# Performance work log

Hardware: AMD Instinct MI355X
Metric: run time of the kernel (lower is better)

The kernel has to match this reference:

```python
import jax, jax.numpy as jnp
import numpy as np

N_EMBED = 1024
HEAD_SIZE = 64
BLOCK_SIZE = 2048

def setup_inputs() -> dict:
    key = jax.random.key(0)
    kx, kq, kk, kv = jax.random.split(key, 4)
    scale = N_EMBED ** -0.5
    x = jax.random.normal(kx, (8, 2048, N_EMBED), dtype=jnp.float32)
    # nn.Linear weights stored as [out, in]; we keep [in, out] for x @ W
    Wq = jax.random.normal(kq, (N_EMBED, HEAD_SIZE), dtype=jnp.float32) * scale
    Wk = jax.random.normal(kk, (N_EMBED, HEAD_SIZE), dtype=jnp.float32) * scale
    Wv = jax.random.normal(kv, (N_EMBED, HEAD_SIZE), dtype=jnp.float32) * scale
    return {"x": x, "Wq": Wq, "Wk": Wk, "Wv": Wv}

def reference(x, Wq, Wk, Wv):
    B, T, C = x.shape
    q = x @ Wq  # [B,T,H]
    k = x @ Wk
    v = x @ Wv
    # NOTE: original scales by C**-0.5 (n_embed), not head_size**-0.5
    wei = jnp.einsum('bth,bsh->bts', q, k) * (C ** -0.5)  # [B,T,T]
    causal = jnp.tril(jnp.ones((T, T), dtype=bool))
    wei = jnp.where(causal, wei, -jnp.inf)
    wei = jax.nn.softmax(wei, axis=-1)
    out = jnp.einsum('bts,bsh->bth', wei, v)  # [B,T,H]
    return out
```

## Files before the change

### kernel.cpp

```cpp
#include <hip/hip_runtime.h>

#define B_ 8
#define T_ 2048
#define C_ 1024
#define H_ 64

typedef __attribute__((ext_vector_type(8))) short short8;
typedef __attribute__((ext_vector_type(4))) float floatx4;
typedef __attribute__((ext_vector_type(4))) int intx4;

static __device__ __forceinline__ unsigned short f2bf(float f) {
  unsigned int u = __builtin_bit_cast(unsigned int, f);
  u += 0x7FFFu + ((u >> 16) & 1u);
  return (unsigned short)(u >> 16);
}
static __device__ __forceinline__ unsigned short f2bf_t(float f) {
  return (unsigned short)(__builtin_bit_cast(unsigned int, f) >> 16);
}
static __device__ __forceinline__ float bf2f(unsigned short u) {
  return __builtin_bit_cast(float, ((unsigned int)u) << 16);
}
static __device__ __forceinline__ unsigned int fbits(float f) {
  return __builtin_bit_cast(unsigned int, f);
}

typedef const __attribute__((address_space(1))) unsigned int* gp1_t;
typedef __attribute__((address_space(3))) unsigned int* lp3_t;
static __device__ __forceinline__ void gl_lds16(const void* g, void* l) {
  __builtin_amdgcn_global_load_lds((gp1_t)g, (lp3_t)l, 16, 0, 0);
}

__global__ __launch_bounds__(256) void conv_w(const float* __restrict__ wq,
    const float* __restrict__ wk, const float* __restrict__ wv,
    unsigned short* __restrict__ wf) {
  int c = blockIdx.x * 256 + threadIdx.x;
  int lane = c & 63;
  int t = c >> 6;
  int ng = t % 12;
  int kk = t / 12;
  int k0 = kk * 32 + (lane >> 4) * 8;
  int n = ng * 16 + (lane & 15);
  const float* src;
  int col;
  float scale = 1.0f;
  if (n < 64)       { src = wq; col = n;       scale = 0.03125f * 1.44269504088896340736f; }
  else if (n < 128) { src = wk; col = n - 64;  }
  else              { src = wv; col = n - 128; }
  unsigned short o[8];
#pragma unroll
  for (int j = 0; j < 8; ++j) o[j] = f2bf(src[(size_t)(k0 + j) * H_ + col] * scale);
  *(uint4*)&wf[(size_t)c * 8] = *(const uint4*)o;
}

__global__ __launch_bounds__(256, 4) void qkv_proj(
    const float* __restrict__ x, const unsigned short* __restrict__ wf,
    unsigned short* __restrict__ qo, unsigned short* __restrict__ kf,
    unsigned short* __restrict__ vf) {
  __shared__ float XL[2][4096];
  int tid = threadIdx.x;
  int wave = tid >> 6, lane = tid & 63;
  int lane4 = lane & 15, quad = lane >> 4;
  int m0 = blockIdx.x * 32;
  int ph0 = blockIdx.x & 7;

  auto stage_ph = [&](int phr, int buf) {
#pragma unroll
    for (int j = 0; j < 4; ++j) {
      int c = (wave * 4 + j) * 64 + lane;
      int r = c >> 5, pc = c & 31;
      int cl = (pc & ~7) | ((pc ^ (r & 7)) & 7);
      gl_lds16(&x[(size_t)(m0 + r) * C_ + phr * 128 + cl * 4], &XL[buf][c * 4]);
    }
  };

  floatx4 acc[2][3];
#pragma unroll
  for (int mt = 0; mt < 2; ++mt)
#pragma unroll
    for (int nt = 0; nt < 3; ++nt) acc[mt][nt] = (floatx4)0.0f;

  stage_ph(ph0, 0);
  __syncthreads();

  for (int ph = 0; ph < 8; ++ph) {
    int buf = ph & 1;
    if (ph < 7) stage_ph((ph + 1 + ph0) & 7, buf ^ 1);
    int phr = (ph + ph0) & 7;
#pragma unroll
    for (int sl = 0; sl < 4; ++sl) {
      int s = phr * 4 + sl;
      short8 b[3];
#pragma unroll
      for (int nt = 0; nt < 3; ++nt)
        b[nt] = *(const short8*)&wf[(size_t)(s * 12 + wave * 3 + nt) * 512 + lane * 8];
      short8 a[2];
#pragma unroll
      for (int mt = 0; mt < 2; ++mt) {
        int r = mt * 16 + lane4;
        int c0 = sl * 8 + quad * 2;
        int pc0 = (c0 & ~7) | ((c0 ^ (r & 7)) & 7);
        int pc1 = ((c0 + 1) & ~7) | (((c0 + 1) ^ (r & 7)) & 7);
        float4 f0 = *(const float4*)&XL[buf][r * 128 + pc0 * 4];
        float4 f1 = *(const float4*)&XL[buf][r * 128 + pc1 * 4];
        intx4 pk;
        pk[0] = (int)__builtin_amdgcn_perm(fbits(f0.y), fbits(f0.x), 0x07060302u);
        pk[1] = (int)__builtin_amdgcn_perm(fbits(f0.w), fbits(f0.z), 0x07060302u);
        pk[2] = (int)__builtin_amdgcn_perm(fbits(f1.y), fbits(f1.x), 0x07060302u);
        pk[3] = (int)__builtin_amdgcn_perm(fbits(f1.w), fbits(f1.z), 0x07060302u);
        a[mt] = __builtin_bit_cast(short8, pk);
      }
#pragma unroll
      for (int mt = 0; mt < 2; ++mt)
#pragma unroll
        for (int nt = 0; nt < 3; ++nt)
          acc[mt][nt] = __builtin_amdgcn_mfma_f32_16x16x32_bf16(a[mt], b[nt], acc[mt][nt], 0, 0, 0);
    }
    __syncthreads();
  }

  unsigned short* VTB = (unsigned short*)&XL[0][0];
  unsigned short* KB  = VTB + 5120;
#pragma unroll
  for (int mt = 0; mt < 2; ++mt)
#pragma unroll
    for (int nt = 0; nt < 3; ++nt) {
      int n = wave * 48 + nt * 16 + lane4;
#pragma unroll
      for (int rr = 0; rr < 4; ++rr) {
        unsigned short val = f2bf(acc[mt][nt][rr]);
        int lrow = mt * 16 + quad * 4 + rr;
        if (n < 64)       qo[(size_t)(m0 + lrow) * H_ + n] = val;
        else if (n < 128) KB[lrow * 72 + (n - 64)] = val;
        else              VTB[(n - 128) * 40 + lrow] = val;
      }
    }
  __syncthreads();
  {
    int bb = m0 >> 11, t0 = m0 & 2047;
    int st = t0 >> 6, off = t0 & 63;
    int ks = tid >> 7, ctl = (tid >> 6) & 1, ln = tid & 63;
    int ct = (off >> 4) + ctl;
    int tl = ctl * 16 + (ln & 15);
    int h0 = ks * 32 + (ln >> 4) * 8;
    uint4 kd = *(const uint4*)&KB[tl * 72 + h0];
    *(uint4*)&kf[((size_t)((bb * 32 + st) * 2 + ks) * 4 + ct) * 512 + ln * 8] = kd;
    int nt = tid >> 6, l4 = tid & 15, qs = (tid >> 4) & 3;
    int ksv = off >> 5;
    uint4 vd = *(const uint4*)&VTB[(nt * 16 + l4) * 40 + qs * 8];
    *(uint4*)&vf[((size_t)((bb * 32 + st) * 2 + ksv) * 4 + nt) * 512 + (tid & 63) * 8] = vd;
  }
}

__global__ __launch_bounds__(256) void attn(
    const unsigned short* __restrict__ qi, const unsigned short* __restrict__ Kf,
    const unsigned short* __restrict__ Vf, unsigned short* __restrict__ Op,
    float* __restrict__ lsum) {
  __shared__ unsigned short PL[4][16][72];

  int tid = threadIdx.x;
  int wave = tid >> 6, lane = tid & 63;
  int lane4 = lane & 15, quad = lane >> 4;
  int qt = 31 - (int)blockIdx.x;
  int b = blockIdx.y, split = blockIdx.z;
  int qb = qt * 64;
  int base = b * T_;

  int ntile = qt + 1;
  int sBeg = (split * ntile) >> 2;
  int sEnd = ((split + 1) * ntile) >> 2;

  short8 aq[2];
#pragma unroll
  for (int ks = 0; ks < 2; ++ks)
    aq[ks] = *(const short8*)&qi[(size_t)(base + qb + wave * 16 + lane4) * H_ + ks * 32 + quad * 8];

  float lrow[4];
  floatx4 o[4];
#pragma unroll
  for (int r = 0; r < 4; ++r) lrow[r] = 0.0f;
#pragma unroll
  for (int nt = 0; nt < 4; ++nt) o[nt] = (floatx4)0.0f;

  for (int st = sBeg; st < sEnd; ++st) {
    size_t tb = (size_t)(b * 32 + st) * 8;
    short8 bk[2][4], bv[2][4];
#pragma unroll
    for (int ks = 0; ks < 2; ++ks)
#pragma unroll
      for (int ct = 0; ct < 4; ++ct)
        bk[ks][ct] = *(const short8*)&Kf[(tb + ks * 4 + ct) * 512 + lane * 8];
#pragma unroll
    for (int ks = 0; ks < 2; ++ks)
#pragma unroll
      for (int nt = 0; nt < 4; ++nt)
        bv[ks][nt] = *(const short8*)&Vf[(tb + ks * 4 + nt) * 512 + lane * 8];

    floatx4 sacc[4];
#pragma unroll
    for (int ct = 0; ct < 4; ++ct) sacc[ct] = (floatx4)0.0f;
#pragma unroll
    for (int ks = 0; ks < 2; ++ks)
#pragma unroll
      for (int ct = 0; ct < 4; ++ct)
        sacc[ct] = __builtin_amdgcn_mfma_f32_16x16x32_bf16(aq[ks], bk[ks][ct], sacc[ct], 0, 0, 0);

    if (st == qt) {
#pragma unroll
      for (int ct = 0; ct < 4; ++ct)
#pragma unroll
        for (int r = 0; r < 4; ++r) {
          int qrow = wave * 16 + quad * 4 + r;
          int scol = ct * 16 + lane4;
          if (scol > qrow) sacc[ct][r] = -3.0e38f;
        }
    }

#pragma unroll
    for (int ct = 0; ct < 4; ++ct)
#pragma unroll
      for (int r = 0; r < 4; ++r) {
        float p = exp2f(sacc[ct][r] - 8.0f);
        lrow[r] += p;
        PL[wave][quad * 4 + r][ct * 16 + lane4] = f2bf_t(p);
      }

#pragma unroll
    for (int ks = 0; ks < 2; ++ks) {
      short8 pa = *(const short8*)&PL[wave][lane4][ks * 32 + quad * 8];
#pragma unroll
      for (int nt = 0; nt < 4; ++nt)
        o[nt] = __builtin_amdgcn_mfma_f32_16x16x32_bf16(pa, bv[ks][nt], o[nt], 0, 0, 0);
    }
  }

#pragma unroll
  for (int off = 1; off < 16; off <<= 1)
#pragma unroll
    for (int r = 0; r < 4; ++r) lrow[r] += __shfl_xor(lrow[r], off);

  size_t pbase = (((size_t)split * 8 + b) * 32 + qt) * 64;
#pragma unroll
  for (int r = 0; r < 4; ++r) {
    int row = wave * 16 + quad * 4 + r;
#pragma unroll
    for (int nt = 0; nt < 4; ++nt)
      Op[(pbase + row) * 64 + nt * 16 + lane4] = f2bf(o[nt][r]);
    if (lane4 == 0) lsum[pbase + row] = lrow[r];
  }
}

__global__ __launch_bounds__(256) void merge_splits(
    const unsigned short* __restrict__ Op, const float* __restrict__ lsum,
    float* __restrict__ out) {
  int idx = blockIdx.x * 256 + threadIdx.x;
  int row = idx >> 4;
  int h4 = (idx & 15) * 4;
  int b = row >> 11, t = row & 2047;
  int qt = t >> 6, r = t & 63;
  float O0 = 0.f, O1 = 0.f, O2 = 0.f, O3 = 0.f, l = 0.f;
#pragma unroll
  for (int s = 0; s < 4; ++s) {
    size_t p = (((size_t)s * 8 + b) * 32 + qt) * 64 + r;
    l += lsum[p];
    ushort4 ov = *(const ushort4*)&Op[p * 64 + h4];
    O0 += bf2f(ov.x); O1 += bf2f(ov.y); O2 += bf2f(ov.z); O3 += bf2f(ov.w);
  }
  float inv = 1.0f / l;
  float4 res = make_float4(O0 * inv, O1 * inv, O2 * inv, O3 * inv);
  *(float4*)&out[(size_t)row * H_ + h4] = res;
}

extern "C" void kernel_launch(void* const* d_in, const int* in_sizes, int n_in,
                              void* d_out, int out_size, void* d_ws, size_t ws_size,
                              hipStream_t stream) {
  const float* x  = (const float*)d_in[0];
  const float* wq = (const float*)d_in[1];
  const float* wk = (const float*)d_in[2];
  const float* wv = (const float*)d_in[3];
  float* out = (float*)d_out;

  char* ws = (char*)d_ws;
  unsigned short* wf = (unsigned short*)ws;
  unsigned short* qb = (unsigned short*)(ws + 393216);
  unsigned short* kf = (unsigned short*)(ws + 2490368);
  unsigned short* vf = (unsigned short*)(ws + 4587520);
  unsigned short* Op = (unsigned short*)(ws + 6684672);
  float*          ls = (float*)(ws + 15073280);

  conv_w<<<96, 256, 0, stream>>>(wq, wk, wv, wf);
  qkv_proj<<<512, 256, 0, stream>>>(x, wf, qb, kf, vf);
  attn<<<dim3(32, 8, 4), 256, 0, stream>>>(qb, kf, vf, Op, ls);
  merge_splits<<<1024, 256, 0, stream>>>(Op, ls, out);
}
```

Measured before the change: 130.3 us.

## Stage K/V tile pairs through LDS with register prefetch in attention

The attention kernel now loads K and V tiles cooperatively across the workgroup into shared memory, two tiles at a time. The next pair is prefetched into registers while the current pair is computed. Previously each wave loaded its own copies straight from global memory. The change also adds s_setprio around the MFMA sections and sets a launch bound of 3 blocks per CU. It adds two barriers per tile pair and more LDS and register pressure, which could reduce occupancy or force spills.

```diff
diff --git a/kernel.cpp b/kernel.cpp
--- a/kernel.cpp
+++ b/kernel.cpp
@@ -151,11 +151,12 @@
   }
 }
 
-__global__ __launch_bounds__(256) void attn(
+__global__ __launch_bounds__(256, 3) void attn(
     const unsigned short* __restrict__ qi, const unsigned short* __restrict__ Kf,
     const unsigned short* __restrict__ Vf, unsigned short* __restrict__ Op,
     float* __restrict__ lsum) {
-  __shared__ unsigned short PL[4][16][72];
+  __shared__ unsigned short KVS[2][8192];
+  __shared__ unsigned short PL[2][4][16][72];
 
   int tid = threadIdx.x;
   int wave = tid >> 6, lane = tid & 63;
@@ -181,28 +182,49 @@
 #pragma unroll
   for (int nt = 0; nt < 4; ++nt) o[nt] = (floatx4)0.0f;
 
-  for (int st = sBeg; st < sEnd; ++st) {
-    size_t tb = (size_t)(b * 32 + st) * 8;
-    short8 bk[2][4], bv[2][4];
+  uint4 rs[8];
+  auto stage_pair = [&](int t0) {
+#pragma unroll
+    for (int half = 0; half < 2; ++half) {
+      int t = t0 + half;
+      if (t < sEnd) {
+#pragma unroll
+        for (int j = 0; j < 4; ++j) {
+          int c = j * 256 + tid;
+          const unsigned short* src = (c < 512)
+              ? &Kf[(size_t)(b * 32 + t) * 4096 + c * 8]
+              : &Vf[(size_t)(b * 32 + t) * 4096 + (size_t)(c - 512) * 8];
+          rs[half * 4 + j] = *(const uint4*)src;
+        }
+      }
+    }
+  };
+  auto write_pair = [&](int t0) {
+#pragma unroll
+    for (int half = 0; half < 2; ++half) {
+      if (t0 + half < sEnd) {
+#pragma unroll
+        for (int j = 0; j < 4; ++j) {
+          int c = j * 256 + tid;
+          *(uint4*)&KVS[half][c * 8] = rs[half * 4 + j];
+        }
+      }
+    }
+  };
+
+  auto tile_compute = [&](int st, int h, int pl) {
+    floatx4 sacc[4];
+#pragma unroll
+    for (int ct = 0; ct < 4; ++ct) sacc[ct] = (floatx4)0.0f;
+    __builtin_amdgcn_s_setprio(1);
 #pragma unroll
     for (int ks = 0; ks < 2; ++ks)
 #pragma unroll
-      for (int ct = 0; ct < 4; ++ct)
-        bk[ks][ct] = *(const short8*)&Kf[(tb + ks * 4 + ct) * 512 + lane * 8];
-#pragma unroll
-    for (int ks = 0; ks < 2; ++ks)
-#pragma unroll
-      for (int nt = 0; nt < 4; ++nt)
-        bv[ks][nt] = *(const short8*)&Vf[(tb + ks * 4 + nt) * 512 + lane * 8];
-
-    floatx4 sacc[4];
-#pragma unroll
-    for (int ct = 0; ct < 4; ++ct) sacc[ct] = (floatx4)0.0f;
-#pragma unroll
-    for (int ks = 0; ks < 2; ++ks)
-#pragma unroll
-      for (int ct = 0; ct < 4; ++ct)
-        sacc[ct] = __builtin_amdgcn_mfma_f32_16x16x32_bf16(aq[ks], bk[ks][ct], sacc[ct], 0, 0, 0);
+      for (int ct = 0; ct < 4; ++ct) {
+        short8 bk = *(const short8*)&KVS[h][(ks * 4 + ct) * 512 + lane * 8];
+        sacc[ct] = __builtin_amdgcn_mfma_f32_16x16x32_bf16(aq[ks], bk, sacc[ct], 0, 0, 0);
+      }
+    __builtin_amdgcn_s_setprio(0);
 
     if (st == qt) {
 #pragma unroll
@@ -221,16 +243,33 @@
       for (int r = 0; r < 4; ++r) {
         float p = exp2f(sacc[ct][r] - 8.0f);
         lrow[r] += p;
-        PL[wave][quad * 4 + r][ct * 16 + lane4] = f2bf_t(p);
-      }
-
+        PL[pl][wave][quad * 4 + r][ct * 16 + lane4] = f2bf_t(p);
+      }
+
+    __builtin_amdgcn_s_setprio(1);
 #pragma unroll
     for (int ks = 0; ks < 2; ++ks) {
-      short8 pa = *(const short8*)&PL[wave][lane4][ks * 32 + quad * 8];
-#pragma unroll
-      for (int nt = 0; nt < 4; ++nt)
-        o[nt] = __builtin_amdgcn_mfma_f32_16x16x32_bf16(pa, bv[ks][nt], o[nt], 0, 0, 0);
-    }
+      short8 pa = *(const short8*)&PL[pl][wave][lane4][ks * 32 + quad * 8];
+#pragma unroll
+      for (int nt = 0; nt < 4; ++nt) {
+        short8 bv = *(const short8*)&KVS[h][4096 + (ks * 4 + nt) * 512 + lane * 8];
+        o[nt] = __builtin_amdgcn_mfma_f32_16x16x32_bf16(pa, bv, o[nt], 0, 0, 0);
+      }
+    }
+    __builtin_amdgcn_s_setprio(0);
+  };
+
+  stage_pair(sBeg);
+  write_pair(sBeg);
+  __syncthreads();
+
+  for (int st = sBeg; st < sEnd; st += 2) {
+    stage_pair(st + 2);
+    tile_compute(st, 0, 0);
+    if (st + 1 < sEnd) tile_compute(st + 1, 1, 1);
+    __syncthreads();
+    write_pair(st + 2);
+    __syncthreads();
   }
 
 #pragma unroll
```

Result: slower. 161.1 us (+23.7%).
